# Performance work log

Measured on AMD Instinct MI355X. Metric: run time of the kernel, lower is better.

The kernel has to match this reference:

```python
import jax, jax.numpy as jnp
import numpy as np

T, B, I, H, O = 512, 64, 256, 512, 256

def setup_inputs() -> dict:
    key = jax.random.key(0)
    ks = jax.random.split(key, 7)
    s_ih = 1.0 / np.sqrt(H)
    return {
        "inputs": jax.random.normal(ks[0], (T, B, I), dtype=jnp.float32),
        "W_ih": jax.random.uniform(ks[1], (4 * H, I), minval=-s_ih, maxval=s_ih, dtype=jnp.float32),
        "W_hh": jax.random.uniform(ks[2], (4 * H, H), minval=-s_ih, maxval=s_ih, dtype=jnp.float32),
        "b_ih": jax.random.uniform(ks[3], (4 * H,), minval=-s_ih, maxval=s_ih, dtype=jnp.float32),
        "b_hh": jax.random.uniform(ks[4], (4 * H,), minval=-s_ih, maxval=s_ih, dtype=jnp.float32),
        "W_out": jax.random.uniform(ks[5], (O, H), minval=-s_ih, maxval=s_ih, dtype=jnp.float32),
        "b_out": jax.random.uniform(ks[6], (O,), minval=-s_ih, maxval=s_ih, dtype=jnp.float32),
    }

def reference(inputs, W_ih, W_hh, b_ih, b_hh, W_out, b_out):
    Bsz = inputs.shape[1]
    Hd = W_hh.shape[1]
    h0 = jnp.zeros((Bsz, Hd), dtype=inputs.dtype)
    c0 = jnp.zeros((Bsz, Hd), dtype=inputs.dtype)
    # Precompute input contribution for all timesteps in one big GEMM: [T,B,4H]
    x_gates = jnp.einsum('tbi,gi->tbg', inputs, W_ih) + b_ih + b_hh

    def step(carry, xg):
        h, c = carry
        gates = xg + h @ W_hh.T  # [B,4H]
        i, f, g, o = jnp.split(gates, 4, axis=-1)  # PyTorch LSTMCell gate order
        i = jax.nn.sigmoid(i)
        f = jax.nn.sigmoid(f)
        g = jnp.tanh(g)
        o = jax.nn.sigmoid(o)
        c_new = f * c + i * g
        h_new = o * jnp.tanh(c_new)
        return (h_new, c_new), h_new

    (h_T, c_T), hs = jax.lax.scan(step, (h0, c0), x_gates)
    # Output projection over all timesteps at once: [T,B,O]
    outputs = jnp.einsum('tbh,oh->tbo', hs, W_out) + b_out
    return (outputs, h_T, c_T)
```

## Files before the change

kernel.cpp:

```cpp
#include <hip/hip_runtime.h>
#include <hip/hip_bf16.h>

#define TLEN 512
#define BATCH 64
#define ISZ 256
#define HSZ 512
#define OSZ 256
#define G4 2048

typedef float f32x4 __attribute__((ext_vector_type(4)));
typedef short short8 __attribute__((ext_vector_type(8)));
typedef int int4v __attribute__((ext_vector_type(4)));

#define MFMA(a, b, c) __builtin_amdgcn_mfma_f32_16x16x32_bf16((a), (b), (c), 0, 0, 0)

__device__ __forceinline__ unsigned short f2bf(float x) {
    unsigned int u = __float_as_uint(x);
    u = (u + 0x7fffu + ((u >> 16) & 1u)) >> 16;
    return (unsigned short)u;
}
__device__ __forceinline__ float bf2f(unsigned short h) {
    return __uint_as_float(((unsigned int)h) << 16);
}
__device__ __forceinline__ float sigmoidf_(float x) { return 1.0f / (1.0f + __expf(-x)); }
__device__ __forceinline__ float tanhf_(float x) { return 1.0f - 2.0f / (__expf(2.0f * x) + 1.0f); }

__global__ void __launch_bounds__(512, 1) xg_gemm(
    const float* __restrict__ inp, const float* __restrict__ Wih,
    const float* __restrict__ b_ih, const float* __restrict__ b_hh,
    unsigned short* __restrict__ xg, int* __restrict__ flags)
{
    __shared__ short8 blds[8][8][64];
    const int tid = threadIdx.x;
    if (blockIdx.x == 0 && blockIdx.y == 0)
        __hip_atomic_store(&flags[tid], 0, __ATOMIC_RELAXED, __HIP_MEMORY_SCOPE_AGENT);
    {
        int row = tid >> 2;
        int kseg = (tid & 3) * 64;
        int nt = row >> 4, nn = row & 15;
        const float* src = Wih + (size_t)(blockIdx.y * 128 + row) * ISZ + kseg;
        for (int kk = 0; kk < 64; ++kk) {
            int k = kseg + kk;
            int kf = k >> 5, sub = k & 31;
            ((unsigned short*)&blds[nt][kf][((sub >> 3) << 4) | nn])[sub & 7] = f2bf(src[kk]);
        }
    }
    __syncthreads();
    const int wave = tid >> 6, lane = tid & 63;
    const int m0 = blockIdx.x * 128 + wave * 16;
    f32x4 acc[8];
    #pragma unroll
    for (int i = 0; i < 8; ++i) acc[i] = (f32x4){0.f, 0.f, 0.f, 0.f};
    const float* arow = inp + (size_t)(m0 + (lane & 15)) * ISZ + ((lane >> 4) * 8);
    #pragma unroll
    for (int kf = 0; kf < 8; ++kf) {
        f32x4 a0 = *(const f32x4*)(arow + kf * 32);
        f32x4 a1 = *(const f32x4*)(arow + kf * 32 + 4);
        short8 af;
        #pragma unroll
        for (int i = 0; i < 4; ++i) { af[i] = (short)f2bf(a0[i]); af[4 + i] = (short)f2bf(a1[i]); }
        #pragma unroll
        for (int nt = 0; nt < 8; ++nt)
            acc[nt] = MFMA(af, blds[nt][kf][lane], acc[nt]);
    }
    const int nn = lane & 15;
    #pragma unroll
    for (int nt = 0; nt < 8; ++nt) {
        int nc = blockIdx.y * 128 + nt * 16 + nn;
        float bias = b_ih[nc] + b_hh[nc];
        #pragma unroll
        for (int r = 0; r < 4; ++r) {
            int m = m0 + (lane >> 4) * 4 + r;
            xg[(size_t)m * G4 + nc] = f2bf(acc[nt][r] + bias);
        }
    }
}

__global__ void __launch_bounds__(256, 1) lstm_scan(
    const float* __restrict__ Whh, const unsigned short* __restrict__ xg,
    unsigned short* __restrict__ hs, unsigned int* __restrict__ hbuf,
    int* __restrict__ flags, float* __restrict__ out_tail)
{
    __shared__ short8 wlds[4][16][64];
    const int wg = blockIdx.x, tid = threadIdx.x;
    const int wave = tid >> 6, lane = tid & 63;
    const int l15 = lane & 15, l4 = lane >> 4;
    const int col = wg * 16 + l15;

    {
        const int g = wave;
        const float* wrow = Whh + (size_t)(g * HSZ + wg * 16 + l15) * HSZ + l4 * 8;
        #pragma unroll
        for (int kf = 0; kf < 16; ++kf) {
            f32x4 w0 = *(const f32x4*)(wrow + kf * 32);
            f32x4 w1 = *(const f32x4*)(wrow + kf * 32 + 4);
            short8 f;
            #pragma unroll
            for (int e = 0; e < 4; ++e) { f[e] = (short)f2bf(w0[e]); f[4 + e] = (short)f2bf(w1[e]); }
            wlds[g][kf][lane] = f;
        }
    }
    __syncthreads();

    float cr[4] = {0.f, 0.f, 0.f, 0.f};
    const int mbase = wave * 16 + l4 * 4;

    #pragma unroll 1
    for (int t = 0; t < TLEN; ++t) {
        float xgf[4][4];
        #pragma unroll
        for (int r = 0; r < 4; ++r) {
            const unsigned short* xrow = xg + (size_t)(t * BATCH + mbase + r) * G4 + col;
            #pragma unroll
            for (int gi = 0; gi < 4; ++gi)
                xgf[gi][r] = bf2f(xrow[gi * HSZ]);
        }

        f32x4 acc[4];
        #pragma unroll
        for (int g = 0; g < 4; ++g) acc[g] = (f32x4){0.f, 0.f, 0.f, 0.f};

        if (t > 0) {
            int fv;
            do {
                fv = (lane < 32)
                   ? __hip_atomic_load(&flags[(wave * 32 + lane) * 4], __ATOMIC_RELAXED, __HIP_MEMORY_SCOPE_AGENT)
                   : t;
            } while (__all(fv >= t) == 0);
            __builtin_amdgcn_sched_barrier(0);
            int4v hhi[16], hlo[16];
            const char* hb  = (const char*)hbuf + (t & 1) * 131072 + (size_t)(wave * 16 + l15) * 1024 + l4 * 16;
            const char* hbl = hb + 65536;
            #pragma unroll
            for (int kf = 0; kf < 16; ++kf) {
                asm volatile("global_load_dwordx4 %0, %1, off offset:%2 sc0 sc1"
                             : "=&v"(hhi[kf]) : "v"(hb),  "i"(kf * 64));
                asm volatile("global_load_dwordx4 %0, %1, off offset:%2 sc0 sc1"
                             : "=&v"(hlo[kf]) : "v"(hbl), "i"(kf * 64));
            }
            asm volatile("s_waitcnt vmcnt(0)" ::: "memory");
            __builtin_amdgcn_sched_barrier(0);
            #pragma unroll
            for (int kf = 0; kf < 16; ++kf) {
                short8 ah = *(short8*)&hhi[kf];
                short8 al = *(short8*)&hlo[kf];
                #pragma unroll
                for (int g = 0; g < 4; ++g) {
                    short8 b = wlds[g][kf][lane];
                    acc[g] = MFMA(ah, b, acc[g]);
                    acc[g] = MFMA(al, b, acc[g]);
                }
            }
        }

        float hnv[4];
        #pragma unroll
        for (int r = 0; r < 4; ++r) {
            float iv = acc[0][r] + xgf[0][r];
            float fv2= acc[1][r] + xgf[1][r];
            float gv = acc[2][r] + xgf[2][r];
            float ov = acc[3][r] + xgf[3][r];
            float si = sigmoidf_(iv), sf = sigmoidf_(fv2), so = sigmoidf_(ov);
            float tg = tanhf_(gv);
            float cn = sf * cr[r] + si * tg;
            cr[r] = cn;
            hnv[r] = so * tanhf_(cn);
        }

        {
            const unsigned int pbase = (unsigned)(((t + 1) & 1) * 32768 + (l15 & 1) * 16384 + wg * 8 + (l15 >> 1));
            #pragma unroll
            for (int r = 0; r < 4; ++r) {
                unsigned int vh = f2bf(hnv[r]);
                unsigned int vl = f2bf(hnv[r] - bf2f((unsigned short)vh));
                unsigned int ph = (unsigned int)__shfl_xor((int)vh, 1);
                unsigned int pl = (unsigned int)__shfl_xor((int)vl, 1);
                unsigned int word = (l15 & 1) ? (pl | (vl << 16)) : (vh | (ph << 16));
                __hip_atomic_store(&hbuf[pbase + (unsigned)(mbase + r) * 256], word,
                                   __ATOMIC_RELAXED, __HIP_MEMORY_SCOPE_AGENT);
            }
        }
        asm volatile("s_waitcnt vmcnt(0)" ::: "memory");
        __builtin_amdgcn_sched_barrier(0);
        if (lane == 0)
            __hip_atomic_store(&flags[(wave * 32 + wg) * 4], t + 1, __ATOMIC_RELAXED, __HIP_MEMORY_SCOPE_AGENT);

        #pragma unroll
        for (int r = 0; r < 4; ++r) {
            int m = mbase + r;
            hs[((size_t)t * BATCH + m) * HSZ + col] = f2bf(hnv[r]);
            if (t == TLEN - 1) {
                out_tail[(size_t)m * HSZ + col] = hnv[r];
                out_tail[(size_t)BATCH * HSZ + (size_t)m * HSZ + col] = cr[r];
            }
        }
    }
}

__global__ void __launch_bounds__(512, 1) out_gemm(
    const unsigned short* __restrict__ hs, const float* __restrict__ Wout,
    const float* __restrict__ b_out, float* __restrict__ out)
{
    __shared__ short8 blds[4][16][64];
    const int tid = threadIdx.x;
    {
        int row = tid >> 3;
        int kseg = (tid & 7) * 64;
        int nt = row >> 4, nn = row & 15;
        const float* src = Wout + (size_t)(blockIdx.y * 64 + row) * HSZ + kseg;
        for (int kk = 0; kk < 64; ++kk) {
            int k = kseg + kk;
            int kf = k >> 5, sub = k & 31;
            ((unsigned short*)&blds[nt][kf][((sub >> 3) << 4) | nn])[sub & 7] = f2bf(src[kk]);
        }
    }
    __syncthreads();
    const int wave = tid >> 6, lane = tid & 63;
    const int m0 = blockIdx.x * 128 + wave * 16;
    f32x4 acc[4];
    #pragma unroll
    for (int i = 0; i < 4; ++i) acc[i] = (f32x4){0.f, 0.f, 0.f, 0.f};
    const unsigned short* arow = hs + (size_t)(m0 + (lane & 15)) * HSZ + ((lane >> 4) * 8);
    #pragma unroll
    for (int kf = 0; kf < 16; ++kf) {
        short8 a = *(const short8*)(arow + kf * 32);
        #pragma unroll
        for (int nt = 0; nt < 4; ++nt)
            acc[nt] = MFMA(a, blds[nt][kf][lane], acc[nt]);
    }
    const int nn = lane & 15;
    #pragma unroll
    for (int nt = 0; nt < 4; ++nt) {
        int nc = blockIdx.y * 64 + nt * 16 + nn;
        float bias = b_out[nc];
        #pragma unroll
        for (int r = 0; r < 4; ++r) {
            int m = m0 + (lane >> 4) * 4 + r;
            out[(size_t)m * OSZ + nc] = acc[nt][r] + bias;
        }
    }
}

extern "C" void kernel_launch(void* const* d_in, const int* in_sizes, int n_in,
                              void* d_out, int out_size, void* d_ws, size_t ws_size,
                              hipStream_t stream)
{
    const float* inputs = (const float*)d_in[0];
    const float* W_ih  = (const float*)d_in[1];
    const float* W_hh  = (const float*)d_in[2];
    const float* b_ih  = (const float*)d_in[3];
    const float* b_hh  = (const float*)d_in[4];
    const float* W_out = (const float*)d_in[5];
    const float* b_out = (const float*)d_in[6];
    float* out = (float*)d_out;

    char* ws = (char*)d_ws;
    unsigned short* xg = (unsigned short*)ws;
    unsigned short* hs = (unsigned short*)(ws + 134217728);
    unsigned int* hbuf = (unsigned int*)(ws + 134217728 + 33554432);
    int* flags         = (int*)(ws + 134217728 + 33554432 + 262144);

    xg_gemm<<<dim3(256, 16), 512, 0, stream>>>(inputs, W_ih, b_ih, b_hh, xg, flags);

    float* out_tail = out + (size_t)TLEN * BATCH * OSZ;
    const float* whh_p = W_hh;
    const unsigned short* xg_p = xg;
    unsigned short* hs_p = hs;
    unsigned int* hbuf_p = hbuf;
    int* flags_p = flags;
    float* tail_p = out_tail;
    void* scan_args[] = { &whh_p, &xg_p, &hs_p, &hbuf_p, &flags_p, &tail_p };
    hipLaunchCooperativeKernel((void*)lstm_scan, dim3(32), dim3(256), scan_args, 0, stream);

    out_gemm<<<dim3(256, 4), 512, 0, stream>>>(hs, W_out, b_out, out);
}
```

Measured before the change: 3.661 ms.

## Fuse step tags into hidden-state words, replacing flag-based LSTM step sync

Each published hidden value now travels in a 32-bit word holding the bf16 value in the upper half and the step index in the lower half. Consumers poll the data itself until every tag matches, which removes the separate flag array, its store and its polling round trip. The error-compensating hi/lo bf16 split of h is dropped, which halves the recurrent MFMAs but loses that extra precision. The xg gate loads are issued as early raw asm loads so they overlap the wait, and the kernel is pinned to one wave per EU.

New measurement: 4.105 ms. 12.1% more time.

```diff
diff --git a/kernel.cpp b/kernel.cpp
--- a/kernel.cpp
+++ b/kernel.cpp
@@ -28,12 +28,10 @@
 __global__ void __launch_bounds__(512, 1) xg_gemm(
     const float* __restrict__ inp, const float* __restrict__ Wih,
     const float* __restrict__ b_ih, const float* __restrict__ b_hh,
-    unsigned short* __restrict__ xg, int* __restrict__ flags)
+    unsigned short* __restrict__ xg)
 {
     __shared__ short8 blds[8][8][64];
     const int tid = threadIdx.x;
-    if (blockIdx.x == 0 && blockIdx.y == 0)
-        __hip_atomic_store(&flags[tid], 0, __ATOMIC_RELAXED, __HIP_MEMORY_SCOPE_AGENT);
     {
         int row = tid >> 2;
         int kseg = (tid & 3) * 64;
@@ -76,10 +74,10 @@
     }
 }
 
-__global__ void __launch_bounds__(256, 1) lstm_scan(
+__global__ void __attribute__((amdgpu_waves_per_eu(1, 1))) __launch_bounds__(256, 1) lstm_scan(
     const float* __restrict__ Whh, const unsigned short* __restrict__ xg,
     unsigned short* __restrict__ hs, unsigned int* __restrict__ hbuf,
-    int* __restrict__ flags, float* __restrict__ out_tail)
+    float* __restrict__ out_tail)
 {
     __shared__ short8 wlds[4][16][64];
     const int wg = blockIdx.x, tid = threadIdx.x;
@@ -107,13 +105,17 @@
 
     #pragma unroll 1
     for (int t = 0; t < TLEN; ++t) {
-        float xgf[4][4];
-        #pragma unroll
-        for (int r = 0; r < 4; ++r) {
-            const unsigned short* xrow = xg + (size_t)(t * BATCH + mbase + r) * G4 + col;
-            #pragma unroll
-            for (int gi = 0; gi < 4; ++gi)
-                xgf[gi][r] = bf2f(xrow[gi * HSZ]);
+        unsigned int xgv[4][4];
+        {
+            const char* x0 = (const char*)(xg + (size_t)(t * BATCH + mbase) * G4 + col);
+            #pragma unroll
+            for (int r = 0; r < 4; ++r) {
+                const char* xr = x0 + r * (G4 * 2);
+                asm volatile("global_load_ushort %0, %1, off offset:0"    : "=v"(xgv[0][r]) : "v"(xr));
+                asm volatile("global_load_ushort %0, %1, off offset:1024" : "=v"(xgv[1][r]) : "v"(xr));
+                asm volatile("global_load_ushort %0, %1, off offset:2048" : "=v"(xgv[2][r]) : "v"(xr));
+                asm volatile("global_load_ushort %0, %1, off offset:3072" : "=v"(xgv[3][r]) : "v"(xr));
+            }
         }
 
         f32x4 acc[4];
@@ -121,45 +123,56 @@
         for (int g = 0; g < 4; ++g) acc[g] = (f32x4){0.f, 0.f, 0.f, 0.f};
 
         if (t > 0) {
-            int fv;
-            do {
-                fv = (lane < 32)
-                   ? __hip_atomic_load(&flags[(wave * 32 + lane) * 4], __ATOMIC_RELAXED, __HIP_MEMORY_SCOPE_AGENT)
-                   : t;
-            } while (__all(fv >= t) == 0);
+            const unsigned tag = (unsigned)t;
+            const char* hb = (const char*)hbuf + (t & 1) * 131072
+                           + (size_t)(wave * 16 + l15) * 2048 + l4 * 32;
+            int4v hv[32];
+            while (true) {
+                #pragma unroll
+                for (int kf = 0; kf < 16; ++kf) {
+                    asm volatile("global_load_dwordx4 %0, %1, off offset:%2 sc0 sc1"
+                                 : "=&v"(hv[2 * kf])     : "v"(hb), "i"(kf * 128));
+                    asm volatile("global_load_dwordx4 %0, %1, off offset:%2 sc0 sc1"
+                                 : "=&v"(hv[2 * kf + 1]) : "v"(hb), "i"(kf * 128 + 16));
+                }
+                asm volatile("s_waitcnt vmcnt(0)" ::: "memory");
+                __builtin_amdgcn_sched_barrier(0);
+                unsigned bad = 0;
+                #pragma unroll
+                for (int w = 0; w < 32; ++w) {
+                    bad |= (unsigned)(hv[w][0] ^ (int)tag);
+                    bad |= (unsigned)(hv[w][1] ^ (int)tag);
+                    bad |= (unsigned)(hv[w][2] ^ (int)tag);
+                    bad |= (unsigned)(hv[w][3] ^ (int)tag);
+                }
+                if (__all((bad & 0xFFFFu) == 0)) break;
+            }
             __builtin_amdgcn_sched_barrier(0);
-            int4v hhi[16], hlo[16];
-            const char* hb  = (const char*)hbuf + (t & 1) * 131072 + (size_t)(wave * 16 + l15) * 1024 + l4 * 16;
-            const char* hbl = hb + 65536;
             #pragma unroll
             for (int kf = 0; kf < 16; ++kf) {
-                asm volatile("global_load_dwordx4 %0, %1, off offset:%2 sc0 sc1"
-                             : "=&v"(hhi[kf]) : "v"(hb),  "i"(kf * 64));
-                asm volatile("global_load_dwordx4 %0, %1, off offset:%2 sc0 sc1"
-                             : "=&v"(hlo[kf]) : "v"(hbl), "i"(kf * 64));
-            }
-            asm volatile("s_waitcnt vmcnt(0)" ::: "memory");
-            __builtin_amdgcn_sched_barrier(0);
-            #pragma unroll
-            for (int kf = 0; kf < 16; ++kf) {
-                short8 ah = *(short8*)&hhi[kf];
-                short8 al = *(short8*)&hlo[kf];
-                #pragma unroll
-                for (int g = 0; g < 4; ++g) {
-                    short8 b = wlds[g][kf][lane];
-                    acc[g] = MFMA(ah, b, acc[g]);
-                    acc[g] = MFMA(al, b, acc[g]);
-                }
-            }
-        }
+                int4v w0 = hv[2 * kf], w1 = hv[2 * kf + 1];
+                int4v f;
+                f[0] = (int)(((unsigned)w0[0] >> 16) | ((unsigned)w0[1] & 0xFFFF0000u));
+                f[1] = (int)(((unsigned)w0[2] >> 16) | ((unsigned)w0[3] & 0xFFFF0000u));
+                f[2] = (int)(((unsigned)w1[0] >> 16) | ((unsigned)w1[1] & 0xFFFF0000u));
+                f[3] = (int)(((unsigned)w1[2] >> 16) | ((unsigned)w1[3] & 0xFFFF0000u));
+                short8 a = *(short8*)&f;
+                acc[0] = MFMA(a, wlds[0][kf][lane], acc[0]);
+                acc[1] = MFMA(a, wlds[1][kf][lane], acc[1]);
+                acc[2] = MFMA(a, wlds[2][kf][lane], acc[2]);
+                acc[3] = MFMA(a, wlds[3][kf][lane], acc[3]);
+            }
+        }
+        asm volatile("s_waitcnt vmcnt(0)" ::: "memory");
+        __builtin_amdgcn_sched_barrier(0);
 
         float hnv[4];
         #pragma unroll
         for (int r = 0; r < 4; ++r) {
-            float iv = acc[0][r] + xgf[0][r];
-            float fv2= acc[1][r] + xgf[1][r];
-            float gv = acc[2][r] + xgf[2][r];
-            float ov = acc[3][r] + xgf[3][r];
+            float iv = acc[0][r] + bf2f((unsigned short)xgv[0][r]);
+            float fv2= acc[1][r] + bf2f((unsigned short)xgv[1][r]);
+            float gv = acc[2][r] + bf2f((unsigned short)xgv[2][r]);
+            float ov = acc[3][r] + bf2f((unsigned short)xgv[3][r]);
             float si = sigmoidf_(iv), sf = sigmoidf_(fv2), so = sigmoidf_(ov);
             float tg = tanhf_(gv);
             float cn = sf * cr[r] + si * tg;
@@ -168,22 +181,15 @@
         }
 
         {
-            const unsigned int pbase = (unsigned)(((t + 1) & 1) * 32768 + (l15 & 1) * 16384 + wg * 8 + (l15 >> 1));
+            const unsigned ptag = (unsigned)(t + 1);
+            const unsigned pbase = ((unsigned)((t + 1) & 1)) * 32768u + (unsigned)col;
             #pragma unroll
             for (int r = 0; r < 4; ++r) {
-                unsigned int vh = f2bf(hnv[r]);
-                unsigned int vl = f2bf(hnv[r] - bf2f((unsigned short)vh));
-                unsigned int ph = (unsigned int)__shfl_xor((int)vh, 1);
-                unsigned int pl = (unsigned int)__shfl_xor((int)vl, 1);
-                unsigned int word = (l15 & 1) ? (pl | (vl << 16)) : (vh | (ph << 16));
-                __hip_atomic_store(&hbuf[pbase + (unsigned)(mbase + r) * 256], word,
+                unsigned word = (((unsigned)f2bf(hnv[r])) << 16) | ptag;
+                __hip_atomic_store(&hbuf[pbase + (unsigned)(mbase + r) * 512], word,
                                    __ATOMIC_RELAXED, __HIP_MEMORY_SCOPE_AGENT);
             }
         }
-        asm volatile("s_waitcnt vmcnt(0)" ::: "memory");
-        __builtin_amdgcn_sched_barrier(0);
-        if (lane == 0)
-            __hip_atomic_store(&flags[(wave * 32 + wg) * 4], t + 1, __ATOMIC_RELAXED, __HIP_MEMORY_SCOPE_AGENT);
 
         #pragma unroll
         for (int r = 0; r < 4; ++r) {
@@ -258,18 +264,16 @@
     unsigned short* xg = (unsigned short*)ws;
     unsigned short* hs = (unsigned short*)(ws + 134217728);
     unsigned int* hbuf = (unsigned int*)(ws + 134217728 + 33554432);
-    int* flags         = (int*)(ws + 134217728 + 33554432 + 262144);
-
-    xg_gemm<<<dim3(256, 16), 512, 0, stream>>>(inputs, W_ih, b_ih, b_hh, xg, flags);
+
+    xg_gemm<<<dim3(256, 16), 512, 0, stream>>>(inputs, W_ih, b_ih, b_hh, xg);
 
     float* out_tail = out + (size_t)TLEN * BATCH * OSZ;
     const float* whh_p = W_hh;
     const unsigned short* xg_p = xg;
     unsigned short* hs_p = hs;
     unsigned int* hbuf_p = hbuf;
-    int* flags_p = flags;
     float* tail_p = out_tail;
-    void* scan_args[] = { &whh_p, &xg_p, &hs_p, &hbuf_p, &flags_p, &tail_p };
+    void* scan_args[] = { &whh_p, &xg_p, &hs_p, &hbuf_p, &tail_p };
     hipLaunchCooperativeKernel((void*)lstm_scan, dim3(32), dim3(256), scan_args, 0, stream);
 
     out_gemm<<<dim3(256, 4), 512, 0, stream>>>(hs, W_out, b_out, out);
```

## Drop bf16 hi/lo split of hidden state and relayout xg for vector loads

Applied to the files above, without the earlier changes.

The recurrent hidden state was previously exchanged as a bf16 hi plus lo pair, with two MFMAs per fragment. It is now exchanged as a single bf16 value, which halves the per-step global loads and the MFMA count on the serial critical path, at the cost of recurrent-matmul precision. The xg buffer is re-laid out per (t, column, gate) so each lane fetches its gate inputs with four dwordx2 loads instead of sixteen scattered ushort loads. Flags are packed densely, and the hs stores are moved before the flag publish so they are covered by the same waitcnt.

Result: faster. 3.286 ms (-10.2%).

```diff
diff --git a/kernel.cpp b/kernel.cpp
--- a/kernel.cpp
+++ b/kernel.cpp
@@ -10,6 +10,7 @@
 
 typedef float f32x4 __attribute__((ext_vector_type(4)));
 typedef short short8 __attribute__((ext_vector_type(8)));
+typedef int int2v __attribute__((ext_vector_type(2)));
 typedef int int4v __attribute__((ext_vector_type(4)));
 
 #define MFMA(a, b, c) __builtin_amdgcn_mfma_f32_16x16x32_bf16((a), (b), (c), 0, 0, 0)
@@ -32,7 +33,7 @@
 {
     __shared__ short8 blds[8][8][64];
     const int tid = threadIdx.x;
-    if (blockIdx.x == 0 && blockIdx.y == 0)
+    if (blockIdx.x == 0 && blockIdx.y == 0 && tid < 128)
         __hip_atomic_store(&flags[tid], 0, __ATOMIC_RELAXED, __HIP_MEMORY_SCOPE_AGENT);
     {
         int row = tid >> 2;
@@ -64,19 +65,21 @@
             acc[nt] = MFMA(af, blds[nt][kf][lane], acc[nt]);
     }
     const int nn = lane & 15;
+    const int mf = m0 + (lane >> 4) * 4;
+    const int tt = mf >> 6, bb = mf & 63;
     #pragma unroll
     for (int nt = 0; nt < 8; ++nt) {
         int nc = blockIdx.y * 128 + nt * 16 + nn;
         float bias = b_ih[nc] + b_hh[nc];
-        #pragma unroll
-        for (int r = 0; r < 4; ++r) {
-            int m = m0 + (lane >> 4) * 4 + r;
-            xg[(size_t)m * G4 + nc] = f2bf(acc[nt][r] + bias);
-        }
-    }
-}
-
-__global__ void __launch_bounds__(256, 1) lstm_scan(
+        int colc = nc & 511, gate = nc >> 9;
+        unsigned lo = (unsigned)f2bf(acc[nt][0] + bias) | ((unsigned)f2bf(acc[nt][1] + bias) << 16);
+        unsigned hi = (unsigned)f2bf(acc[nt][2] + bias) | ((unsigned)f2bf(acc[nt][3] + bias) << 16);
+        int2v w; w[0] = (int)lo; w[1] = (int)hi;
+        *(int2v*)((char*)xg + (size_t)(tt * 512 + colc) * 512 + gate * 128 + bb * 2) = w;
+    }
+}
+
+__global__ void __attribute__((amdgpu_waves_per_eu(1, 1))) __launch_bounds__(256, 1) lstm_scan(
     const float* __restrict__ Whh, const unsigned short* __restrict__ xg,
     unsigned short* __restrict__ hs, unsigned int* __restrict__ hbuf,
     int* __restrict__ flags, float* __restrict__ out_tail)
@@ -107,59 +110,79 @@
 
     #pragma unroll 1
     for (int t = 0; t < TLEN; ++t) {
-        float xgf[4][4];
-        #pragma unroll
-        for (int r = 0; r < 4; ++r) {
-            const unsigned short* xrow = xg + (size_t)(t * BATCH + mbase + r) * G4 + col;
-            #pragma unroll
-            for (int gi = 0; gi < 4; ++gi)
-                xgf[gi][r] = bf2f(xrow[gi * HSZ]);
+        int2v xv[4];
+        {
+            const char* xb = (const char*)xg + (size_t)(t * 512 + col) * 512 + mbase * 2;
+            asm volatile(
+                "global_load_dwordx2 %0, %4, off offset:0\n\t"
+                "global_load_dwordx2 %1, %4, off offset:128\n\t"
+                "global_load_dwordx2 %2, %4, off offset:256\n\t"
+                "global_load_dwordx2 %3, %4, off offset:384"
+                : "=&v"(xv[0]), "=&v"(xv[1]), "=&v"(xv[2]), "=&v"(xv[3])
+                : "v"(xb) : "memory");
         }
 
         f32x4 acc[4];
         #pragma unroll
         for (int g = 0; g < 4; ++g) acc[g] = (f32x4){0.f, 0.f, 0.f, 0.f};
 
+        int4v hv[16];
         if (t > 0) {
+            const int idx = wave * 32 + (lane & 31);
             int fv;
             do {
-                fv = (lane < 32)
-                   ? __hip_atomic_load(&flags[(wave * 32 + lane) * 4], __ATOMIC_RELAXED, __HIP_MEMORY_SCOPE_AGENT)
-                   : t;
+                fv = __hip_atomic_load(&flags[idx], __ATOMIC_RELAXED, __HIP_MEMORY_SCOPE_AGENT);
             } while (__all(fv >= t) == 0);
             __builtin_amdgcn_sched_barrier(0);
-            int4v hhi[16], hlo[16];
-            const char* hb  = (const char*)hbuf + (t & 1) * 131072 + (size_t)(wave * 16 + l15) * 1024 + l4 * 16;
-            const char* hbl = hb + 65536;
+            const char* hb = (const char*)hbuf + (t & 1) * 65536
+                           + (size_t)(wave * 16 + l15) * 1024 + l4 * 16;
+            asm volatile(
+                "global_load_dwordx4 %0, %16, off offset:0 sc0 sc1\n\t"
+                "global_load_dwordx4 %1, %16, off offset:64 sc0 sc1\n\t"
+                "global_load_dwordx4 %2, %16, off offset:128 sc0 sc1\n\t"
+                "global_load_dwordx4 %3, %16, off offset:192 sc0 sc1\n\t"
+                "global_load_dwordx4 %4, %16, off offset:256 sc0 sc1\n\t"
+                "global_load_dwordx4 %5, %16, off offset:320 sc0 sc1\n\t"
+                "global_load_dwordx4 %6, %16, off offset:384 sc0 sc1\n\t"
+                "global_load_dwordx4 %7, %16, off offset:448 sc0 sc1\n\t"
+                "global_load_dwordx4 %8, %16, off offset:512 sc0 sc1\n\t"
+                "global_load_dwordx4 %9, %16, off offset:576 sc0 sc1\n\t"
+                "global_load_dwordx4 %10, %16, off offset:640 sc0 sc1\n\t"
+                "global_load_dwordx4 %11, %16, off offset:704 sc0 sc1\n\t"
+                "global_load_dwordx4 %12, %16, off offset:768 sc0 sc1\n\t"
+                "global_load_dwordx4 %13, %16, off offset:832 sc0 sc1\n\t"
+                "global_load_dwordx4 %14, %16, off offset:896 sc0 sc1\n\t"
+                "global_load_dwordx4 %15, %16, off offset:960 sc0 sc1"
+                : "=&v"(hv[0]), "=&v"(hv[1]), "=&v"(hv[2]), "=&v"(hv[3]),
+                  "=&v"(hv[4]), "=&v"(hv[5]), "=&v"(hv[6]), "=&v"(hv[7]),
+                  "=&v"(hv[8]), "=&v"(hv[9]), "=&v"(hv[10]), "=&v"(hv[11]),
+                  "=&v"(hv[12]), "=&v"(hv[13]), "=&v"(hv[14]), "=&v"(hv[15])
+                : "v"(hb) : "memory");
+        }
+        asm volatile("s_waitcnt vmcnt(0)" ::: "memory");
+        __builtin_amdgcn_sched_barrier(0);
+
+        if (t > 0) {
             #pragma unroll
             for (int kf = 0; kf < 16; ++kf) {
-                asm volatile("global_load_dwordx4 %0, %1, off offset:%2 sc0 sc1"
-                             : "=&v"(hhi[kf]) : "v"(hb),  "i"(kf * 64));
-                asm volatile("global_load_dwordx4 %0, %1, off offset:%2 sc0 sc1"
-                             : "=&v"(hlo[kf]) : "v"(hbl), "i"(kf * 64));
+                short8 a = *(short8*)&hv[kf];
+                acc[0] = MFMA(a, wlds[0][kf][lane], acc[0]);
+                acc[1] = MFMA(a, wlds[1][kf][lane], acc[1]);
+                acc[2] = MFMA(a, wlds[2][kf][lane], acc[2]);
+                acc[3] = MFMA(a, wlds[3][kf][lane], acc[3]);
             }
-            asm volatile("s_waitcnt vmcnt(0)" ::: "memory");
-            __builtin_amdgcn_sched_barrier(0);
-            #pragma unroll
-            for (int kf = 0; kf < 16; ++kf) {
-                short8 ah = *(short8*)&hhi[kf];
-                short8 al = *(short8*)&hlo[kf];
-                #pragma unroll
-                for (int g = 0; g < 4; ++g) {
-                    short8 b = wlds[g][kf][lane];
-                    acc[g] = MFMA(ah, b, acc[g]);
-                    acc[g] = MFMA(al, b, acc[g]);
-                }
-            }
         }
 
         float hnv[4];
         #pragma unroll
         for (int r = 0; r < 4; ++r) {
-            float iv = acc[0][r] + xgf[0][r];
-            float fv2= acc[1][r] + xgf[1][r];
-            float gv = acc[2][r] + xgf[2][r];
-            float ov = acc[3][r] + xgf[3][r];
+            unsigned w0 = (unsigned)xv[0][r >> 1], w1 = (unsigned)xv[1][r >> 1];
+            unsigned w2 = (unsigned)xv[2][r >> 1], w3 = (unsigned)xv[3][r >> 1];
+            int sh = (r & 1) * 16;
+            float iv = acc[0][r] + bf2f((unsigned short)(w0 >> sh));
+            float fv2= acc[1][r] + bf2f((unsigned short)(w1 >> sh));
+            float gv = acc[2][r] + bf2f((unsigned short)(w2 >> sh));
+            float ov = acc[3][r] + bf2f((unsigned short)(w3 >> sh));
             float si = sigmoidf_(iv), sf = sigmoidf_(fv2), so = sigmoidf_(ov);
             float tg = tanhf_(gv);
             float cn = sf * cr[r] + si * tg;
@@ -168,32 +191,33 @@
         }
 
         {
-            const unsigned int pbase = (unsigned)(((t + 1) & 1) * 32768 + (l15 & 1) * 16384 + wg * 8 + (l15 >> 1));
+            const unsigned pbase = ((unsigned)((t + 1) & 1)) * 16384u + (unsigned)(col >> 1);
             #pragma unroll
             for (int r = 0; r < 4; ++r) {
-                unsigned int vh = f2bf(hnv[r]);
-                unsigned int vl = f2bf(hnv[r] - bf2f((unsigned short)vh));
-                unsigned int ph = (unsigned int)__shfl_xor((int)vh, 1);
-                unsigned int pl = (unsigned int)__shfl_xor((int)vl, 1);
-                unsigned int word = (l15 & 1) ? (pl | (vl << 16)) : (vh | (ph << 16));
-                __hip_atomic_store(&hbuf[pbase + (unsigned)(mbase + r) * 256], word,
-                                   __ATOMIC_RELAXED, __HIP_MEMORY_SCOPE_AGENT);
+                unsigned v = f2bf(hnv[r]);
+                unsigned p = (unsigned)__shfl_xor((int)v, 1);
+                if ((l15 & 1) == 0)
+                    __hip_atomic_store(&hbuf[pbase + (unsigned)(mbase + r) * 256], v | (p << 16),
+                                       __ATOMIC_RELAXED, __HIP_MEMORY_SCOPE_AGENT);
+            }
+        }
+        #pragma unroll
+        for (int r = 0; r < 4; ++r) {
+            int m = mbase + r;
+            hs[((size_t)t * BATCH + m) * HSZ + col] = f2bf(hnv[r]);
+        }
+        if (t == TLEN - 1) {
+            #pragma unroll
+            for (int r = 0; r < 4; ++r) {
+                int m = mbase + r;
+                out_tail[(size_t)m * HSZ + col] = hnv[r];
+                out_tail[(size_t)BATCH * HSZ + (size_t)m * HSZ + col] = cr[r];
             }
         }
         asm volatile("s_waitcnt vmcnt(0)" ::: "memory");
         __builtin_amdgcn_sched_barrier(0);
         if (lane == 0)
-            __hip_atomic_store(&flags[(wave * 32 + wg) * 4], t + 1, __ATOMIC_RELAXED, __HIP_MEMORY_SCOPE_AGENT);
-
-        #pragma unroll
-        for (int r = 0; r < 4; ++r) {
-            int m = mbase + r;
-            hs[((size_t)t * BATCH + m) * HSZ + col] = f2bf(hnv[r]);
-            if (t == TLEN - 1) {
-                out_tail[(size_t)m * HSZ + col] = hnv[r];
-                out_tail[(size_t)BATCH * HSZ + (size_t)m * HSZ + col] = cr[r];
-            }
-        }
+            __hip_atomic_store(&flags[wave * 32 + wg], t + 1, __ATOMIC_RELAXED, __HIP_MEMORY_SCOPE_AGENT);
     }
 }
 
@@ -258,7 +282,7 @@
     unsigned short* xg = (unsigned short*)ws;
     unsigned short* hs = (unsigned short*)(ws + 134217728);
     unsigned int* hbuf = (unsigned int*)(ws + 134217728 + 33554432);
-    int* flags         = (int*)(ws + 134217728 + 33554432 + 262144);
+    int* flags         = (int*)(ws + 134217728 + 33554432 + 131072);
 
     xg_gemm<<<dim3(256, 16), 512, 0, stream>>>(inputs, W_ih, b_ih, b_hh, xg, flags);
 
```
